# Kernel optimization log

Measured on AMD Instinct MI355X. Metric: run time of the kernel, lower is better.

Reference implementation:

```python
import jax, jax.numpy as jnp
import numpy as np
import math

B, S, D, H = 8, 1024, 512, 8
AD = D // H  # attn_dim = 64


def setup_inputs() -> dict:
    key = jax.random.key(0)
    ks = jax.random.split(key, 16)
    def lin(i):
        w = jax.random.normal(ks[i], (D, D), jnp.float32) * (1.0 / math.sqrt(D))
        b = jnp.zeros((D,), jnp.float32)
        return w, b
    Wq, bq = lin(0); Wk, bk = lin(1); Wv, bv = lin(2); Wr, br = lin(3); Wo, bo = lin(4)
    return {
        "query": jax.random.normal(ks[5], (B, S, D), jnp.float32),
        "key": jax.random.normal(ks[6], (B, S, D), jnp.float32),
        "value": jax.random.normal(ks[7], (B, S, D), jnp.float32),
        "relpos": jax.random.normal(ks[8], (B, S, D), jnp.float32),
        "key_padding_mask": jnp.zeros((B, S), dtype=bool),
        "Wq": Wq, "bq": bq, "Wk": Wk, "bk": bk, "Wv": Wv, "bv": bv,
        "Wr": Wr, "br": br, "Wo": Wo, "bo": bo,
        "U_bias": jax.random.normal(ks[9], (H, AD), jnp.float32) * 0.05,
        "V_bias": jax.random.normal(ks[10], (H, AD), jnp.float32) * 0.05,
    }


def _rel_shift(x):
    # x: (b, h, q, k). Transformer-XL shift trick.
    b, h, q, k = x.shape
    xp = jnp.pad(x, ((0, 0), (0, 0), (0, 0), (1, 0)))  # (b,h,q,k+1)
    xp = xp.reshape(b, h, k + 1, q)
    return xp[:, :, 1:].reshape(b, h, q, k)


def reference(query, key, value, relpos, key_padding_mask,
              Wq, bq, Wk, bk, Wv, bv, Wr, br, Wo, bo, U_bias, V_bias):
    b = query.shape[0]
    Q = (query @ Wq.T + bq).reshape(b, -1, H, AD)    # (b,q,h,d)
    K = (key @ Wk.T + bk).reshape(b, -1, H, AD)      # (b,k,h,d)
    V = (value @ Wv.T + bv).reshape(b, -1, H, AD)    # (b,k,h,d)
    R = (relpos @ Wr.T + br).reshape(b, -1, H, AD)   # (b,k,h,d)

    AC = jnp.einsum('bqhd,bkhd->bhqk', Q + U_bias, K)
    BD = _rel_shift(jnp.einsum('bqhd,bkhd->bhqk', Q + V_bias, R))
    scores = (AC + BD) / math.sqrt(AD)               # (b,h,q,k)

    bias = jnp.where(key_padding_mask, jnp.float32(-1e9), jnp.float32(0.0))
    scores = scores + bias[:, None, None, :]
    attn = jax.nn.softmax(scores, axis=-1)           # (b,h,q,k)

    Hc = jnp.einsum('bhqk,bkhd->bqhd', attn, V).reshape(b, -1, D)
    out = Hc @ Wo.T + bo
    attn_weights = attn.reshape(b * H, attn.shape[2], attn.shape[3])
    return out, attn_weights
```

## Files before the change

### kernel.cpp

```cpp
#include <hip/hip_runtime.h>


typedef __attribute__((ext_vector_type(8))) short bf16x8;
typedef __attribute__((ext_vector_type(8))) float f32x8;
typedef __attribute__((ext_vector_type(4))) float f32x4;

#define MFMA16(a, b, c) __builtin_amdgcn_mfma_f32_16x16x32_bf16((a), (b), (c), 0, 0, 0)

__device__ __forceinline__ float b2f(short s) {
    union { unsigned u; float f; } v;
    v.u = ((unsigned)(unsigned short)s) << 16;
    return v.f;
}
__device__ __forceinline__ short f2b(float f) {
    union { float f; unsigned u; } v;
    v.f = f;
    unsigned r = v.u + 0x7fffu + ((v.u >> 16) & 1u);
    return (short)(r >> 16);
}
__device__ __forceinline__ bf16x8 ld8(const void* p, long idx, int isbf) {
    if (isbf) return *(const bf16x8*)((const short*)p + idx);
    f32x8 f = *(const f32x8*)((const float*)p + idx);
    bf16x8 r;
#pragma unroll
    for (int j = 0; j < 8; j++) r[j] = f2b(f[j]);
    return r;
}
__device__ __forceinline__ float ld1(const void* p, long idx, int isbf) {
    return isbf ? b2f(((const short*)p)[idx]) : ((const float*)p)[idx];
}

__global__ void sniff_dtype(const unsigned* __restrict__ q, int* __restrict__ flag) {
    if (threadIdx.x == 0 && blockIdx.x == 0) {
        int hits = 0;
        for (int i = 0; i < 64; i++) {
            unsigned e = (q[i] >> 7) & 0xFFu;
            hits += (e >= 100u && e <= 140u) ? 1 : 0;
        }
        *flag = (hits > 40) ? 1 : 0;
    }
}

struct CvtArgs { const void* src[8]; };
__global__ __launch_bounds__(256) void convert_all(
        CvtArgs a, short* __restrict__ dst, const int* __restrict__ flag) {
    const int isbf = *flag;
    const long NP = 4194304, WN = 262144;
    const int bid = blockIdx.x;
    int seg;
    long dstoff, eoff;
    if (bid < 8192) {
        seg = bid >> 11;
        dstoff = (long)seg * NP;
        eoff = (long)(bid & 2047) * 2048 + threadIdx.x * 8;
    } else {
        seg = 4 + ((bid - 8192) >> 7);
        dstoff = 4 * NP + (long)(seg - 4) * WN;
        eoff = (long)((bid - 8192) & 127) * 2048 + threadIdx.x * 8;
    }
    const void* s = a.src[seg];
    if (isbf) {
        *(bf16x8*)(dst + dstoff + eoff) = *(const bf16x8*)((const short*)s + eoff);
    } else {
        f32x8 f = *(const f32x8*)((const float*)s + eoff);
        bf16x8 r;
#pragma unroll
        for (int j = 0; j < 8; j++) r[j] = f2b(f[j]);
        *(bf16x8*)(dst + dstoff + eoff) = r;
    }
}

__device__ __forceinline__ void gemm_body(
        const short* __restrict__ A, const void* __restrict__ W,
        const void* __restrict__ bias, void* __restrict__ C,
        int bm, int bn, int isbf, int w_isbf, int c_f32) {
    const int w = threadIdx.x >> 6, lane = threadIdx.x & 63;
    const int m0 = bm * 128 + (w >> 1) * 64;
    const int n0 = bn * 128 + (w & 1) * 64;
    const int lr = lane & 15, lk8 = (lane >> 4) * 8;

    f32x4 acc[4][4] = {};
    for (int kk = 0; kk < 512; kk += 32) {
        bf16x8 a[4], bfr[4];
#pragma unroll
        for (int r = 0; r < 4; r++)
            a[r] = *(const bf16x8*)(A + (long)(m0 + r * 16 + lr) * 512 + kk + lk8);
#pragma unroll
        for (int c = 0; c < 4; c++)
            bfr[c] = ld8(W, (long)(n0 + c * 16 + lr) * 512 + kk + lk8, w_isbf);
#pragma unroll
        for (int r = 0; r < 4; r++)
#pragma unroll
            for (int c = 0; c < 4; c++)
                acc[r][c] = MFMA16(a[r], bfr[c], acc[r][c]);
    }
    const int orow = (lane >> 4) * 4;
#pragma unroll
    for (int c = 0; c < 4; c++) {
        const int col = n0 + c * 16 + lr;
        const float bv = ld1(bias, col, isbf);
#pragma unroll
        for (int r = 0; r < 4; r++)
#pragma unroll
            for (int j = 0; j < 4; j++) {
                const long off = (long)(m0 + r * 16 + orow + j) * 512 + col;
                const float v = acc[r][c][j] + bv;
                if (c_f32) ((float*)C)[off] = v;
                else       ((short*)C)[off] = f2b(v);
            }
    }
}

__global__ __launch_bounds__(256) void gemm_xwT(
        const short* __restrict__ A, const void* __restrict__ W,
        const void* __restrict__ bias, void* __restrict__ C,
        const int* __restrict__ flag, int w_dyn, int c_f32) {
    const int isbf = *flag;
    gemm_body(A, W, bias, C, blockIdx.x & 63, blockIdx.x >> 6,
              isbf, w_dyn ? isbf : 1, c_f32);
}

struct P4 { const void* bias[4]; short* C[4]; };
__global__ __launch_bounds__(256) void proj4(
        const short* __restrict__ Sc, P4 p4, const int* __restrict__ flag) {
    const int isbf = *flag;
    const long NP = 4194304, WN = 262144;
    const int p = blockIdx.x;
    const int xcd = p & 7, u = p >> 3;
    const int op = xcd >> 1;
    const int idx = (xcd & 1) * 128 + u;
    gemm_body(Sc + (long)op * NP, Sc + 4 * NP + (long)op * WN,
              p4.bias[op], p4.C[op], idx & 63, idx >> 6, isbf, 1, 0);
}

__global__ __launch_bounds__(256) void transpose_v(
        const short* __restrict__ Vp, short* __restrict__ Vt) {
    __shared__ short T[64][72];
    const int bh = blockIdx.x >> 2;
    const int kq = blockIdx.x & 3;
    const int b = bh >> 3, h = bh & 7;
    const int t = threadIdx.x;
    const short* src = Vp + (long)b * 1024 * 512 + h * 64;
    short* dst = Vt + (long)bh * 65536;
    for (int kb = kq * 4; kb < kq * 4 + 4; kb++) {
        __syncthreads();
#pragma unroll
        for (int it = 0; it < 2; it++) {
            const int row = it * 32 + (t >> 3);
            const int col = (t & 7) * 8;
            *(bf16x8*)&T[row][col] =
                *(const bf16x8*)(src + (long)(kb * 64 + row) * 512 + col);
        }
        __syncthreads();
#pragma unroll
        for (int it = 0; it < 2; it++) {
            const int d = it * 32 + (t >> 3);
            const int kk = (t & 7) * 8;
            bf16x8 v;
#pragma unroll
            for (int e = 0; e < 8; e++) v[e] = T[kk + e][d];
            *(bf16x8*)(dst + (long)d * 1024 + kb * 64 + kk) = v;
        }
    }
}

__global__ __launch_bounds__(256, 4) void attn_fused(
        const short* __restrict__ Q, const short* __restrict__ K,
        const short* __restrict__ R, const short* __restrict__ Vt,
        const void* __restrict__ Ub, const void* __restrict__ Vb,
        const unsigned char* __restrict__ mask,
        float* __restrict__ attn_out, short* __restrict__ Hc,
        const int* __restrict__ flag) {
    __shared__ __align__(16) short Esh[17 * 1032];
    __shared__ float redmx[4][16];
    __shared__ float redsm[4][16];
    const int isbf = *flag;

    const int p = blockIdx.x;
    const int xcd = p & 7, u = p >> 3;
    const int bh = (u >> 6) * 8 + xcd;
    const int qt = u & 63;
    const int b = bh >> 3, h = bh & 7;
    const int q0 = qt * 16;
    const int w = threadIdx.x >> 6, lane = threadIdx.x & 63;
    const int lr = lane & 15, lg = lane >> 4, lk8 = lg * 8;

    const long kvbase = (long)(b * 1024) * 512 + h * 64;

    {
        bf16x8 aV0[2], aV1[2];
#pragma unroll
        for (int ks = 0; ks < 2; ks++) {
            const int dof = ks * 32 + lk8;
            bf16x8 qv = *(const bf16x8*)(Q + (long)(b * 1024 + q0 + lr) * 512 + h * 64 + dof);
            int qr = q0 + 16 + lr;
            if (qr > 1023) qr = 1023;
            bf16x8 qv1 = *(const bf16x8*)(Q + (long)(b * 1024 + qr) * 512 + h * 64 + dof);
#pragma unroll
            for (int j = 0; j < 8; j++) {
                const float vbj = ld1(Vb, h * 64 + dof + j, isbf);
                aV0[ks][j] = f2b(b2f(qv[j]) + vbj);
                aV1[ks][j] = f2b(b2f(qv1[j]) + vbj);
            }
        }
        for (int tt = 0; tt < 16; tt++) {
            const int k0 = (w * 16 + tt) * 16;
            f32x4 e0 = {}, e1 = {};
#pragma unroll
            for (int ks = 0; ks < 2; ks++) {
                bf16x8 rf = *(const bf16x8*)(R + kvbase + (long)(k0 + lr) * 512 + ks * 32 + lk8);
                e0 = MFMA16(aV0[ks], rf, e0);
                e1 = MFMA16(aV1[ks], rf, e1);
            }
            const int jcol = k0 + lr;
#pragma unroll
            for (int j = 0; j < 4; j++)
                Esh[(lg * 4 + j) * 1032 + jcol] = f2b(e0[j]);
            if (lg == 0) Esh[16 * 1032 + jcol] = f2b(e1[0]);
        }
    }
    __syncthreads();

    f32x4 acc[16];
    {
        bf16x8 aU[2];
#pragma unroll
        for (int ks = 0; ks < 2; ks++) {
            const int dof = ks * 32 + lk8;
            bf16x8 qv = *(const bf16x8*)(Q + (long)(b * 1024 + q0 + lr) * 512 + h * 64 + dof);
#pragma unroll
            for (int j = 0; j < 8; j++)
                aU[ks][j] = f2b(b2f(qv[j]) + ld1(Ub, h * 64 + dof + j, isbf));
        }
        const unsigned char* mrow = mask + b * 1024;
#pragma unroll
        for (int tt = 0; tt < 16; tt++) {
            const int k0 = (w * 16 + tt) * 16;
            f32x4 a = {};
#pragma unroll
            for (int ks = 0; ks < 2; ks++) {
                bf16x8 kf = *(const bf16x8*)(K + kvbase + (long)(k0 + lr) * 512 + ks * 32 + lk8);
                a = MFMA16(aU[ks], kf, a);
            }
            const int c = k0 + lr;
            const float mbias = mrow[c] ? -1e9f : 0.0f;
#pragma unroll
            for (int j = 0; j < 4; j++) {
                const int r = lg * 4 + j;
                const int dq = c - q0 - r;
                const int idx = r * 1032 + dq + ((dq <= 0) ? 1023 : 1030);
                float bd = b2f(Esh[idx]);
                if (dq == 1) bd = 0.0f;
                a[j] = (a[j] + bd) * 0.125f + mbias;
            }
            acc[tt] = a;
        }
    }

    float mx[4], sm[4];
#pragma unroll
    for (int j = 0; j < 4; j++) {
        float m = -1e30f;
#pragma unroll
        for (int tt = 0; tt < 16; tt++) m = fmaxf(m, acc[tt][j]);
#pragma unroll
        for (int off = 1; off <= 8; off <<= 1) m = fmaxf(m, __shfl_xor(m, off));
        mx[j] = m;
    }
    if (lr == 0) {
#pragma unroll
        for (int j = 0; j < 4; j++) redmx[w][lg * 4 + j] = mx[j];
    }
    __syncthreads();
#pragma unroll
    for (int j = 0; j < 4; j++) {
        float m = redmx[0][lg * 4 + j];
#pragma unroll
        for (int ww = 1; ww < 4; ww++) m = fmaxf(m, redmx[ww][lg * 4 + j]);
        mx[j] = m;
        sm[j] = 0.0f;
    }
#pragma unroll
    for (int tt = 0; tt < 16; tt++)
#pragma unroll
        for (int j = 0; j < 4; j++) {
            const float e = __expf(acc[tt][j] - mx[j]);
            acc[tt][j] = e;
            sm[j] += e;
        }
#pragma unroll
    for (int j = 0; j < 4; j++) {
        float s = sm[j];
#pragma unroll
        for (int off = 1; off <= 8; off <<= 1) s += __shfl_xor(s, off);
        sm[j] = s;
    }
    if (lr == 0) {
#pragma unroll
        for (int j = 0; j < 4; j++) redsm[w][lg * 4 + j] = sm[j];
    }
    __syncthreads();
    float inv[4];
#pragma unroll
    for (int j = 0; j < 4; j++) {
        float s = redsm[0][lg * 4 + j];
#pragma unroll
        for (int ww = 1; ww < 4; ww++) s += redsm[ww][lg * 4 + j];
        inv[j] = 1.0f / s;
    }

    short* P = Esh;
#pragma unroll
    for (int tt = 0; tt < 16; tt++) {
        const int c = (w * 16 + tt) * 16 + lr;
#pragma unroll
        for (int j = 0; j < 4; j++)
            P[(lg * 4 + j) * 1048 + c] = f2b(acc[tt][j] * inv[j]);
    }
    __syncthreads();

    float* abase = attn_out + ((long)bh * 1024 + q0) * 1024;
#pragma unroll
    for (int rr = 0; rr < 4; rr++) {
        const int r = w * 4 + rr;
#pragma unroll
        for (int half = 0; half < 2; half++) {
            const bf16x8 pv8 = *(const bf16x8*)&P[r * 1048 + half * 512 + lane * 8];
            f32x4 lo, hi;
#pragma unroll
            for (int e = 0; e < 4; e++) { lo[e] = b2f(pv8[e]); hi[e] = b2f(pv8[4 + e]); }
            float* dst = abase + (long)r * 1024 + half * 512 + lane * 8;
            *(f32x4*)dst = lo;
            *(f32x4*)(dst + 4) = hi;
        }
    }

    f32x4 oacc = {};
    const short* vtb = Vt + (long)bh * 65536 + (long)(w * 16 + lr) * 1024;
    for (int ks = 0; ks < 32; ks++) {
        const bf16x8 aa = *(const bf16x8*)&P[lr * 1048 + ks * 32 + lk8];
        const bf16x8 bb = *(const bf16x8*)(vtb + ks * 32 + lk8);
        oacc = MFMA16(aa, bb, oacc);
    }
#pragma unroll
    for (int j = 0; j < 4; j++)
        Hc[(long)(b * 1024 + q0 + lg * 4 + j) * 512 + h * 64 + w * 16 + lr] = f2b(oacc[j]);
}

extern "C" void kernel_launch(void* const* d_in, const int* in_sizes, int n_in,
                              void* d_out, int out_size, void* d_ws, size_t ws_size,
                              hipStream_t stream) {
    const void* query  = d_in[0];
    const void* key    = d_in[1];
    const void* value  = d_in[2];
    const void* relpos = d_in[3];
    const unsigned char* mask = (const unsigned char*)d_in[4];
    const void* Wq = d_in[5];  const void* bq = d_in[6];
    const void* Wk = d_in[7];  const void* bk = d_in[8];
    const void* Wv = d_in[9];  const void* bv = d_in[10];
    const void* Wr = d_in[11]; const void* br = d_in[12];
    const void* Wo = d_in[13]; const void* bo = d_in[14];
    const void* Ub = d_in[15]; const void* Vb = d_in[16];

    float* out  = (float*)d_out;
    float* attn = out + (long)4194304;

    const long NP = 4194304;
    short* ws = (short*)d_ws;
    short* Kp = ws;
    short* Vp = ws + NP;
    short* Rp = ws + 2 * NP;
    int* flag = (int*)(ws + 3 * NP);
    short* Qp = (short*)out;
    short* Vt = (short*)out + NP;
    short* Hc = Vp;
    short* Sc = (short*)attn;

    sniff_dtype<<<1, 64, 0, stream>>>((const unsigned*)query, flag);

    CvtArgs ca;
    ca.src[0] = query; ca.src[1] = key; ca.src[2] = value; ca.src[3] = relpos;
    ca.src[4] = Wq; ca.src[5] = Wk; ca.src[6] = Wv; ca.src[7] = Wr;
    convert_all<<<8704, 256, 0, stream>>>(ca, Sc, flag);

    P4 p4;
    p4.bias[0] = bq; p4.C[0] = Qp;
    p4.bias[1] = bk; p4.C[1] = Kp;
    p4.bias[2] = bv; p4.C[2] = Vp;
    p4.bias[3] = br; p4.C[3] = Rp;
    proj4<<<1024, 256, 0, stream>>>(Sc, p4, flag);

    transpose_v<<<256, 256, 0, stream>>>(Vp, Vt);

    attn_fused<<<4096, 256, 0, stream>>>(Qp, Kp, Rp, Vt, Ub, Vb, mask,
                                         attn, Hc, flag);

    gemm_xwT<<<256, 256, 0, stream>>>(Hc, Wo, bo, out, flag, 1, 1);
}
```

Baseline: 365.3 us.

## Fuse BD and AC score loops, merge softmax reductions, store attn directly

Merges the R-projection (BD) and K-projection (AC) MFMA loops into a single pass, issuing the K and R loads together so there is more memory parallelism. The softmax now makes one cross-wave reduction pass: each wave keeps a local max and sum, and they are combined with an exp rescale. This removes one __syncthreads and one shared-memory round trip. The attention probabilities are written to global memory as full-precision fp32 with nontemporal stores straight from registers, instead of being read back as bf16 from LDS, which trades the previous coalesced 16-byte vector stores for scattered scalar 4-byte stores. Register pressure rises because the aU/aV fragments and acc are all live at once.

```diff
diff --git a/kernel.cpp b/kernel.cpp
--- a/kernel.cpp
+++ b/kernel.cpp
@@ -187,77 +187,64 @@
 
     const long kvbase = (long)(b * 1024) * 512 + h * 64;
 
-    {
-        bf16x8 aV0[2], aV1[2];
-#pragma unroll
-        for (int ks = 0; ks < 2; ks++) {
-            const int dof = ks * 32 + lk8;
-            bf16x8 qv = *(const bf16x8*)(Q + (long)(b * 1024 + q0 + lr) * 512 + h * 64 + dof);
-            int qr = q0 + 16 + lr;
-            if (qr > 1023) qr = 1023;
-            bf16x8 qv1 = *(const bf16x8*)(Q + (long)(b * 1024 + qr) * 512 + h * 64 + dof);
-#pragma unroll
-            for (int j = 0; j < 8; j++) {
-                const float vbj = ld1(Vb, h * 64 + dof + j, isbf);
-                aV0[ks][j] = f2b(b2f(qv[j]) + vbj);
-                aV1[ks][j] = f2b(b2f(qv1[j]) + vbj);
-            }
-        }
-        for (int tt = 0; tt < 16; tt++) {
-            const int k0 = (w * 16 + tt) * 16;
-            f32x4 e0 = {}, e1 = {};
-#pragma unroll
-            for (int ks = 0; ks < 2; ks++) {
-                bf16x8 rf = *(const bf16x8*)(R + kvbase + (long)(k0 + lr) * 512 + ks * 32 + lk8);
-                e0 = MFMA16(aV0[ks], rf, e0);
-                e1 = MFMA16(aV1[ks], rf, e1);
-            }
-            const int jcol = k0 + lr;
-#pragma unroll
-            for (int j = 0; j < 4; j++)
-                Esh[(lg * 4 + j) * 1032 + jcol] = f2b(e0[j]);
-            if (lg == 0) Esh[16 * 1032 + jcol] = f2b(e1[0]);
-        }
+    bf16x8 aU[2], aV0[2], aV1[2];
+#pragma unroll
+    for (int ks = 0; ks < 2; ks++) {
+        const int dof = ks * 32 + lk8;
+        bf16x8 qv = *(const bf16x8*)(Q + (long)(b * 1024 + q0 + lr) * 512 + h * 64 + dof);
+        int qr = q0 + 16 + lr;
+        if (qr > 1023) qr = 1023;
+        bf16x8 qv1 = *(const bf16x8*)(Q + (long)(b * 1024 + qr) * 512 + h * 64 + dof);
+#pragma unroll
+        for (int j = 0; j < 8; j++) {
+            const float ubj = ld1(Ub, h * 64 + dof + j, isbf);
+            const float vbj = ld1(Vb, h * 64 + dof + j, isbf);
+            const float qf = b2f(qv[j]);
+            aU[ks][j]  = f2b(qf + ubj);
+            aV0[ks][j] = f2b(qf + vbj);
+            aV1[ks][j] = f2b(b2f(qv1[j]) + vbj);
+        }
+    }
+
+    f32x4 acc[16];
+#pragma unroll 4
+    for (int tt = 0; tt < 16; tt++) {
+        const int k0 = (w * 16 + tt) * 16;
+        const long rowb = kvbase + (long)(k0 + lr) * 512;
+        bf16x8 rf0 = *(const bf16x8*)(R + rowb + lk8);
+        bf16x8 rf1 = *(const bf16x8*)(R + rowb + 32 + lk8);
+        bf16x8 kf0 = *(const bf16x8*)(K + rowb + lk8);
+        bf16x8 kf1 = *(const bf16x8*)(K + rowb + 32 + lk8);
+        f32x4 e0 = {}, e1 = {}, a = {};
+        e0 = MFMA16(aV0[0], rf0, e0); e0 = MFMA16(aV0[1], rf1, e0);
+        e1 = MFMA16(aV1[0], rf0, e1); e1 = MFMA16(aV1[1], rf1, e1);
+        a  = MFMA16(aU[0],  kf0, a);  a  = MFMA16(aU[1],  kf1, a);
+        const int jcol = k0 + lr;
+#pragma unroll
+        for (int j = 0; j < 4; j++)
+            Esh[(lg * 4 + j) * 1032 + jcol] = f2b(e0[j]);
+        if (lg == 0) Esh[16 * 1032 + jcol] = f2b(e1[0]);
+        acc[tt] = a;
     }
     __syncthreads();
 
-    f32x4 acc[16];
-    {
-        bf16x8 aU[2];
-#pragma unroll
-        for (int ks = 0; ks < 2; ks++) {
-            const int dof = ks * 32 + lk8;
-            bf16x8 qv = *(const bf16x8*)(Q + (long)(b * 1024 + q0 + lr) * 512 + h * 64 + dof);
-#pragma unroll
-            for (int j = 0; j < 8; j++)
-                aU[ks][j] = f2b(b2f(qv[j]) + ld1(Ub, h * 64 + dof + j, isbf));
-        }
-        const unsigned char* mrow = mask + b * 1024;
-#pragma unroll
-        for (int tt = 0; tt < 16; tt++) {
-            const int k0 = (w * 16 + tt) * 16;
-            f32x4 a = {};
-#pragma unroll
-            for (int ks = 0; ks < 2; ks++) {
-                bf16x8 kf = *(const bf16x8*)(K + kvbase + (long)(k0 + lr) * 512 + ks * 32 + lk8);
-                a = MFMA16(aU[ks], kf, a);
-            }
-            const int c = k0 + lr;
-            const float mbias = mrow[c] ? -1e9f : 0.0f;
-#pragma unroll
-            for (int j = 0; j < 4; j++) {
-                const int r = lg * 4 + j;
-                const int dq = c - q0 - r;
-                const int idx = r * 1032 + dq + ((dq <= 0) ? 1023 : 1030);
-                float bd = b2f(Esh[idx]);
-                if (dq == 1) bd = 0.0f;
-                a[j] = (a[j] + bd) * 0.125f + mbias;
-            }
-            acc[tt] = a;
-        }
-    }
-
-    float mx[4], sm[4];
+    const unsigned char* mrow = mask + b * 1024;
+#pragma unroll
+    for (int tt = 0; tt < 16; tt++) {
+        const int c = (w * 16 + tt) * 16 + lr;
+        const float mbias = mrow[c] ? -1e9f : 0.0f;
+#pragma unroll
+        for (int j = 0; j < 4; j++) {
+            const int r = lg * 4 + j;
+            const int dq = c - q0 - r;
+            const int idx = r * 1032 + dq + ((dq <= 0) ? 1023 : 1030);
+            float bd = b2f(Esh[idx]);
+            if (dq == 1) bd = 0.0f;
+            acc[tt][j] = (acc[tt][j] + bd) * 0.125f + mbias;
+        }
+    }
+
+    float mxl[4], sml[4];
 #pragma unroll
     for (int j = 0; j < 4; j++) {
         float m = -1e30f;
@@ -265,75 +252,58 @@
         for (int tt = 0; tt < 16; tt++) m = fmaxf(m, acc[tt][j]);
 #pragma unroll
         for (int off = 1; off <= 8; off <<= 1) m = fmaxf(m, __shfl_xor(m, off));
-        mx[j] = m;
+        mxl[j] = m;
+        sml[j] = 0.0f;
+    }
+#pragma unroll
+    for (int tt = 0; tt < 16; tt++)
+#pragma unroll
+        for (int j = 0; j < 4; j++) {
+            const float e = __expf(acc[tt][j] - mxl[j]);
+            acc[tt][j] = e;
+            sml[j] += e;
+        }
+#pragma unroll
+    for (int j = 0; j < 4; j++) {
+#pragma unroll
+        for (int off = 1; off <= 8; off <<= 1) sml[j] += __shfl_xor(sml[j], off);
     }
     if (lr == 0) {
 #pragma unroll
-        for (int j = 0; j < 4; j++) redmx[w][lg * 4 + j] = mx[j];
+        for (int j = 0; j < 4; j++) {
+            redmx[w][lg * 4 + j] = mxl[j];
+            redsm[w][lg * 4 + j] = sml[j];
+        }
     }
     __syncthreads();
+    float scale[4];
 #pragma unroll
     for (int j = 0; j < 4; j++) {
-        float m = redmx[0][lg * 4 + j];
-#pragma unroll
-        for (int ww = 1; ww < 4; ww++) m = fmaxf(m, redmx[ww][lg * 4 + j]);
-        mx[j] = m;
-        sm[j] = 0.0f;
-    }
-#pragma unroll
-    for (int tt = 0; tt < 16; tt++)
-#pragma unroll
-        for (int j = 0; j < 4; j++) {
-            const float e = __expf(acc[tt][j] - mx[j]);
-            acc[tt][j] = e;
-            sm[j] += e;
-        }
-#pragma unroll
-    for (int j = 0; j < 4; j++) {
-        float s = sm[j];
-#pragma unroll
-        for (int off = 1; off <= 8; off <<= 1) s += __shfl_xor(s, off);
-        sm[j] = s;
-    }
-    if (lr == 0) {
-#pragma unroll
-        for (int j = 0; j < 4; j++) redsm[w][lg * 4 + j] = sm[j];
-    }
-    __syncthreads();
-    float inv[4];
-#pragma unroll
-    for (int j = 0; j < 4; j++) {
-        float s = redsm[0][lg * 4 + j];
-#pragma unroll
-        for (int ww = 1; ww < 4; ww++) s += redsm[ww][lg * 4 + j];
-        inv[j] = 1.0f / s;
+        const int r = lg * 4 + j;
+        float mg = redmx[0][r];
+#pragma unroll
+        for (int ww = 1; ww < 4; ww++) mg = fmaxf(mg, redmx[ww][r]);
+        float sg = 0.0f;
+#pragma unroll
+        for (int ww = 0; ww < 4; ww++)
+            sg += redsm[ww][r] * __expf(redmx[ww][r] - mg);
+        scale[j] = __expf(mxl[j] - mg) / sg;
     }
 
     short* P = Esh;
+    float* abase = attn_out + ((long)bh * 1024 + q0) * 1024;
 #pragma unroll
     for (int tt = 0; tt < 16; tt++) {
         const int c = (w * 16 + tt) * 16 + lr;
 #pragma unroll
-        for (int j = 0; j < 4; j++)
-            P[(lg * 4 + j) * 1048 + c] = f2b(acc[tt][j] * inv[j]);
+        for (int j = 0; j < 4; j++) {
+            const int r = lg * 4 + j;
+            const float pv = acc[tt][j] * scale[j];
+            P[r * 1048 + c] = f2b(pv);
+            __builtin_nontemporal_store(pv, abase + (long)r * 1024 + c);
+        }
     }
     __syncthreads();
-
-    float* abase = attn_out + ((long)bh * 1024 + q0) * 1024;
-#pragma unroll
-    for (int rr = 0; rr < 4; rr++) {
-        const int r = w * 4 + rr;
-#pragma unroll
-        for (int half = 0; half < 2; half++) {
-            const bf16x8 pv8 = *(const bf16x8*)&P[r * 1048 + half * 512 + lane * 8];
-            f32x4 lo, hi;
-#pragma unroll
-            for (int e = 0; e < 4; e++) { lo[e] = b2f(pv8[e]); hi[e] = b2f(pv8[4 + e]); }
-            float* dst = abase + (long)r * 1024 + half * 512 + lane * 8;
-            *(f32x4*)dst = lo;
-            *(f32x4*)(dst + 4) = hi;
-        }
-    }
 
     f32x4 oacc = {};
     const short* vtb = Vt + (long)bh * 65536 + (long)(w * 16 + lr) * 1024;
```

New measurement: 500.6 us. 37.0% more time.
